# Kernel tuning notes

Hardware: AMD Instinct MI355X
Metric: run time of the kernel (lower is better)

## Reference

```python
import jax, jax.numpy as jnp
import numpy as np

V = 28   # len(string.ascii_lowercase + ' #')
D = 32   # embed dim
H = 2    # heads
DH = D // H
B = 64
S = 1024


def _pe(seq_len, d):
    pos = np.arange(seq_len, dtype=np.float32)[:, None]
    div = np.exp(np.arange(0, d, 2, dtype=np.float32) * (-np.log(10000.0) / d))
    pe = np.zeros((seq_len, d), np.float32)
    pe[:, 0::2] = np.sin(pos * div)
    pe[:, 1::2] = np.cos(pos * div)
    return jnp.asarray(pe)


def setup_inputs() -> dict:
    key = jax.random.key(0)
    ks = jax.random.split(key, 12)
    x = jax.random.randint(ks[0], (B, S), 0, V)
    # per-row valid length in [1, S-4] so last 1-index + 3 stays in range (as original assumes)
    lengths = jax.random.randint(ks[1], (B,), 1, S - 3)
    mask = (jnp.arange(S)[None, :] < lengths[:, None]).astype(jnp.float32)[..., None]
    sc = 1.0 / np.sqrt(D)
    emb = jax.random.normal(ks[2], (V, D), jnp.float32)
    wq = jax.random.normal(ks[3], (D, D), jnp.float32) * sc
    wk = jax.random.normal(ks[4], (D, D), jnp.float32) * sc
    wv = jax.random.normal(ks[5], (D, D), jnp.float32) * sc
    bq = jnp.zeros((D,), jnp.float32)
    bk = jnp.zeros((D,), jnp.float32)
    bv = jnp.zeros((D,), jnp.float32)
    wo = jax.random.normal(ks[6], (D, D), jnp.float32) * sc
    bo = jnp.zeros((D,), jnp.float32)
    w_fc = jax.random.normal(ks[7], (V, D), jnp.float32) * sc
    b_fc = jnp.zeros((V,), jnp.float32)
    pe = _pe(S, D)
    return {"x": x, "mask": mask, "emb": emb, "pe": pe,
            "wq": wq, "bq": bq, "wk": wk, "bk": bk, "wv": wv, "bv": bv,
            "wo": wo, "bo": bo, "w_fc": w_fc, "b_fc": b_fc}


def reference(x, mask, emb, pe, wq, bq, wk, bk, wv, bv, wo, bo, w_fc, b_fc):
    Bn, Sn = x.shape
    h = emb[x] + pe[:Sn]                      # [B,S,D]
    m = mask[..., 0]                          # [B,S]
    # vectorized "last valid index" (replaces per-row python loop + .item())
    valid = m > 0
    last = Sn - 1 - jnp.argmax(valid[:, ::-1], axis=1)   # [B]
    pos = jnp.arange(Sn)
    ext = (pos[None, :] > last[:, None]) & (pos[None, :] <= last[:, None] + 3) \
          & (last[:, None] < Sn - 1)
    nm = jnp.where(ext, jnp.float32(1.0), m)  # extended mask [B,S]
    h = h * nm[..., None]
    # multihead self-attention (torch MultiheadAttention, batch_first)
    def heads(t):
        return t.reshape(Bn, Sn, H, DH).transpose(0, 2, 1, 3)  # [B,H,S,DH]
    q = heads(h @ wq.T + bq)
    k = heads(h @ wk.T + bk)
    v = heads(h @ wv.T + bv)
    scores = jnp.einsum('bhqd,bhkd->bhqk', q, k) / jnp.sqrt(jnp.float32(DH))
    scores = jnp.where((nm == 0)[:, None, None, :], jnp.float32(-1e9), scores)
    a = jax.nn.softmax(scores, axis=-1)
    o = jnp.einsum('bhqk,bhkd->bhqd', a, v).transpose(0, 2, 1, 3).reshape(Bn, Sn, D)
    o = o @ wo.T + bo
    return o @ w_fc.T + b_fc                  # [B,S,V]
```

## Files before the change

kernel.cpp:

```cpp
#include <hip/hip_runtime.h>
#include <math.h>

#define BB 64
#define SS 1024
#define DD 32
#define HH 2
#define DHH 16
#define VV 28
#define QSC 0.3606737602222409f

typedef __attribute__((ext_vector_type(8))) short bf16x8;
typedef __attribute__((ext_vector_type(4))) float f32x4;

__device__ __forceinline__ unsigned pack_hi2(float a, float b) {
    return __builtin_amdgcn_perm(__float_as_uint(b), __float_as_uint(a), 0x07060302u);
}
__device__ __forceinline__ float trunc_hi(float a) {
    return __uint_as_float(__float_as_uint(a) & 0xFFFF0000u);
}
__device__ __forceinline__ unsigned bf_rtne_u(float x) {
    unsigned u = __float_as_uint(x);
    return (u + 0x7FFFu + ((u >> 16) & 1u)) >> 16;
}
__device__ __forceinline__ unsigned pack_rtne2(float a, float b) {
    return bf_rtne_u(a) | (bf_rtne_u(b) << 16);
}
__device__ __forceinline__ bf16x8 as_bf16x8(uint4 u) {
    union { uint4 u; bf16x8 v; } cv; cv.u = u; return cv.v;
}


__global__ __launch_bounds__(256) void k_pre(
        const int* __restrict__ x, const float* __restrict__ mask,
        const float* __restrict__ emb, const float* __restrict__ pe,
        const float* __restrict__ wq, const float* __restrict__ bq,
        const float* __restrict__ wk, const float* __restrict__ bk,
        const float* __restrict__ wv, const float* __restrict__ bv,
        const float* __restrict__ wo, const float* __restrict__ bo,
        const float* __restrict__ wfc, const float* __restrict__ bfc,
        int* __restrict__ e, float* __restrict__ W2, float* __restrict__ b2,
        char* __restrict__ qf, char* __restrict__ kf, char* __restrict__ vf) {
    int bid = blockIdx.x;
    int tid = threadIdx.x;
    if (bid < 1024) {
        __shared__ __align__(16) char hbuf[10240];
        __shared__ __align__(16) float Cb[4][16 * 17];
        char* hHi = hbuf;
        char* hLo = hbuf + 5120;
        int wave = tid >> 6, lane = tid & 63;
        int c = lane & 15, kq = lane >> 4;
        {
            int tt = tid >> 2, q4 = tid & 3;
            int idx = bid * 64 + tt;
            int b = idx >> 10, s = idx & 1023;
            float nm = (mask[b * SS + (s >= 3 ? s - 3 : 0)] != 0.0f) ? 1.0f : 0.0f;
            int tok = x[idx];
            float h[8];
#pragma unroll
            for (int i = 0; i < 8; i++)
                h[i] = (emb[tok * DD + q4 * 8 + i] + pe[s * DD + q4 * 8 + i]) * nm;
            unsigned wh[4], wl[4];
#pragma unroll
            for (int wd = 0; wd < 4; wd++) {
                float a0 = h[2 * wd], a1 = h[2 * wd + 1];
                wh[wd] = pack_hi2(a0, a1);
                wl[wd] = pack_hi2(a0 - trunc_hi(a0), a1 - trunc_hi(a1));
            }
            *(uint4*)(hHi + tt * 80 + q4 * 16) = uint4{wh[0], wh[1], wh[2], wh[3]};
            *(uint4*)(hLo + tt * 80 + q4 * 16) = uint4{wl[0], wl[1], wl[2], wl[3]};
        }
        __syncthreads();
        bf16x8 aHh, aHl;
        {
            int off = (wave * 16 + c) * 80 + kq * 16;
            aHh = *(const bf16x8*)(hHi + off);
            aHl = *(const bf16x8*)(hLo + off);
        }
        int blk_b = bid >> 4;
        int s_w = ((bid * 64) & 1023) + wave * 16;
        const f32x4 z4 = {0.0f, 0.0f, 0.0f, 0.0f};
#pragma unroll
        for (int M = 0; M < 3; M++) {
            const float* W    = M == 0 ? wq : (M == 1 ? wk : wv);
            const float* bias = M == 0 ? bq : (M == 1 ? bk : bv);
            bf16x8 Bh[2], Bl[2];
            float bv_[2];
#pragma unroll
            for (int nt = 0; nt < 2; nt++) {
                const float* wrow = W + (nt * 16 + c) * DD + kq * 8;
                float4 wa = ((const float4*)wrow)[0];
                float4 wb = ((const float4*)wrow)[1];
                float f[8] = {wa.x, wa.y, wa.z, wa.w, wb.x, wb.y, wb.z, wb.w};
                unsigned uh[4], ul[4];
#pragma unroll
                for (int wd = 0; wd < 4; wd++) {
                    float a0 = f[2 * wd], a1 = f[2 * wd + 1];
                    uh[wd] = pack_hi2(a0, a1);
                    ul[wd] = pack_hi2(a0 - trunc_hi(a0), a1 - trunc_hi(a1));
                }
                Bh[nt] = as_bf16x8(uint4{uh[0], uh[1], uh[2], uh[3]});
                Bl[nt] = as_bf16x8(uint4{ul[0], ul[1], ul[2], ul[3]});
                bv_[nt] = bias[nt * 16 + c];
            }
#pragma unroll
            for (int nt = 0; nt < 2; nt++) {
                f32x4 acc = __builtin_amdgcn_mfma_f32_16x16x32_bf16(aHh, Bh[nt], z4, 0, 0, 0);
                acc = __builtin_amdgcn_mfma_f32_16x16x32_bf16(aHl, Bh[nt], acc, 0, 0, 0);
                acc = __builtin_amdgcn_mfma_f32_16x16x32_bf16(aHh, Bl[nt], acc, 0, 0, 0);
#pragma unroll
                for (int r = 0; r < 4; r++) {
                    float val = acc[r] + bv_[nt];
                    if (M == 0) val *= QSC;
                    Cb[wave][(kq * 4 + r) * 17 + c] = val;
                }
                int bh = blk_b * 2 + nt;
                if (M == 0) {
                    int tile = s_w >> 4;
                    int qd = lane >> 4, cc = lane & 15;
                    float f[8];
#pragma unroll
                    for (int j = 0; j < 8; j++) f[j] = Cb[wave][cc * 17 + (qd & 1) * 8 + j];
                    unsigned u[4];
                    if (qd < 2) {
#pragma unroll
                        for (int wd = 0; wd < 4; wd++) u[wd] = pack_hi2(f[2 * wd], f[2 * wd + 1]);
                    } else {
#pragma unroll
                        for (int wd = 0; wd < 4; wd++) {
                            float a0 = f[2 * wd] - trunc_hi(f[2 * wd]);
                            float a1 = f[2 * wd + 1] - trunc_hi(f[2 * wd + 1]);
                            u[wd] = pack_hi2(a0, a1);
                        }
                    }
                    *(uint4*)(qf + ((size_t)((bh << 6) + tile) << 10) + lane * 16)
                        = uint4{u[0], u[1], u[2], u[3]};
                } else if (M == 1) {
                    int cl = lane & 3, qd = (lane >> 2) & 3, t = lane >> 4;
                    int ch = s_w >> 7, g1 = (s_w >> 6) & 1, c0 = (s_w & 63) >> 2;
                    int keyl = 4 * cl + t;
                    float f[8];
#pragma unroll
                    for (int j = 0; j < 8; j++) f[j] = Cb[wave][keyl * 17 + (qd & 1) * 8 + j];
                    unsigned uh[4];
#pragma unroll
                    for (int wd = 0; wd < 4; wd++) uh[wd] = pack_rtne2(f[2 * wd], f[2 * wd + 1]);
                    char* base = kf + ((size_t)((bh << 3) + ch) << 13)
                               + ((g1 << 2) + t) * 1024 + qd * 256 + (c0 + cl) * 16;
                    *(uint4*)(base) = uint4{uh[0], uh[1], uh[2], uh[3]};
                } else if (lane < 32) {
                    int gg = (s_w >> 6) & 15, Qs = (s_w >> 4) & 3;
                    int qrel = lane >> 4, dh = lane & 15;
                    unsigned u[4];
#pragma unroll
                    for (int wd = 0; wd < 4; wd++) {
                        float f0 = Cb[wave][(qrel * 8 + 2 * wd) * 17 + dh];
                        float f1 = Cb[wave][(qrel * 8 + 2 * wd + 1) * 17 + dh];
                        u[wd] = pack_rtne2(f0, f1);
                    }
                    *(uint4*)(vf + ((size_t)((bh << 5) + (gg << 1) + qrel) << 10)
                              + (Qs * 16 + dh) * 16)
                        = uint4{u[0], u[1], u[2], u[3]};
                }
            }
        }
    } else if (bid < 1088) {
        int b = bid - 1024;
        int lm = -1;
        for (int s = tid; s < SS; s += 256)
            if (mask[b * SS + s] != 0.0f) lm = s;
        __shared__ int red[256];
        red[tid] = lm;
        __syncthreads();
        for (int off = 128; off > 0; off >>= 1) {
            if (tid < off) red[tid] = max(red[tid], red[tid + off]);
            __syncthreads();
        }
        if (tid == 0) {
            int last = red[0];
            int ee = last;
            if (last < SS - 1) ee = min(last + 3, SS - 1);
            e[b] = ee;
        }
    } else {
        for (int t2 = tid; t2 < VV * DD + VV; t2 += 256) {
            if (t2 < VV * DD) {
                int vv = t2 / DD, i = t2 % DD;
                float a = 0.0f;
                for (int j = 0; j < DD; j++) a += wfc[vv * DD + j] * wo[j * DD + i];
                W2[t2] = a;
            } else {
                int vv = t2 - VV * DD;
                float a = bfc[vv];
                for (int j = 0; j < DD; j++) a += wfc[vv * DD + j] * bo[j];
                b2[vv] = a;
            }
        }
    }
}

__global__ __launch_bounds__(256) void k_attn_fc(
        const char* __restrict__ qf, const char* __restrict__ kf,
        const char* __restrict__ vf, const int* __restrict__ e,
        const float* __restrict__ W2, const float* __restrict__ b2,
        float* __restrict__ out) {
    __shared__ __align__(16) float Ob[32 * 36];
    __shared__ __align__(16) float sW[VV * 36];
    __shared__ float sb[VV];
    int tid = threadIdx.x;
    int f = blockIdx.x + (blockIdx.y << 5);
    int b = ((f & 7) << 3) + ((f >> 3) & 7);
    int qt = f >> 6;

    for (int i = tid; i < VV * DD; i += 256) sW[(i >> 5) * 36 + (i & 31)] = W2[i];
    if (tid < VV) sb[tid] = b2[tid];

    int kmax = e[b] + 1;
    int ng = (kmax + 63) >> 6;

    int wave = tid >> 6, lane = tid & 63, quad = lane >> 4, c = lane & 15;
    int h = wave & 1, ts = wave >> 1;
    int tile = (qt << 1) + ts;
    int bh = b * 2 + h;

    const char* kbase = kf + ((size_t)(bh << 3) << 13);
    const char* vbase = vf + ((size_t)bh << 15);

    bf16x8 aQ = *(const bf16x8*)(qf + ((size_t)((bh << 6) + tile) << 10) + lane * 16);
    const f32x4 z4 = {0.0f, 0.0f, 0.0f, 0.0f};
    f32x4 accO = z4;
    float l_ = 0.0f;

    for (int g = 0; g < ng; g++) {
        const char* kg = kbase + (size_t)g * 4096;
        const char* vg = vbase + (size_t)g * 2048;
        bf16x8 bv0 = *(const bf16x8*)(vg + lane * 16);
        bf16x8 bv1 = *(const bf16x8*)(vg + 1024 + lane * 16);
        f32x4 st[4];
#pragma unroll
        for (int t = 0; t < 4; t++) {
            bf16x8 aK = *(const bf16x8*)(kg + t * 1024 + lane * 16);
            st[t] = __builtin_amdgcn_mfma_f32_16x16x32_bf16(aK, aQ, z4, 0, 0, 0);
        }
        if (((g + 1) << 6) > kmax) {
            int kb = (g << 6) + (quad << 4);
#pragma unroll
            for (int t = 0; t < 4; t++)
#pragma unroll
                for (int r = 0; r < 4; r++)
                    if (kb + 4 * r + t >= kmax) st[t][r] = -3e38f;
        }
        float p[4][4];
#pragma unroll
        for (int t = 0; t < 4; t++)
#pragma unroll
            for (int r = 0; r < 4; r++) p[t][r] = exp2f(st[t][r]);
#pragma unroll
        for (int t = 0; t < 4; t++)
            l_ += (p[t][0] + p[t][1]) + (p[t][2] + p[t][3]);
        bf16x8 pa0 = as_bf16x8(uint4{pack_hi2(p[0][0], p[1][0]), pack_hi2(p[2][0], p[3][0]),
                                     pack_hi2(p[0][1], p[1][1]), pack_hi2(p[2][1], p[3][1])});
        bf16x8 pa1 = as_bf16x8(uint4{pack_hi2(p[0][2], p[1][2]), pack_hi2(p[2][2], p[3][2]),
                                     pack_hi2(p[0][3], p[1][3]), pack_hi2(p[2][3], p[3][3])});
        accO = __builtin_amdgcn_mfma_f32_16x16x32_bf16(pa0, bv0, accO, 0, 0, 0);
        accO = __builtin_amdgcn_mfma_f32_16x16x32_bf16(pa1, bv1, accO, 0, 0, 0);
    }

    l_ += __shfl_xor(l_, 16);
    l_ += __shfl_xor(l_, 32);

    float* obr = Ob + (ts * 16 + quad * 4) * 36 + h * 16 + c;
#pragma unroll
    for (int r = 0; r < 4; r++) {
        float lr = __shfl(l_, (quad << 2) + r, 16);
        obr[r * 36] = accO[r] * __builtin_amdgcn_rcpf(lr);
    }
    __syncthreads();

    int rl = tid >> 3, j = tid & 7;
    if (j < 7) {
        const float* orow = Ob + rl * 36;
        float ov[DD];
#pragma unroll
        for (int i = 0; i < DD; i += 4) {
            float4 t4 = *(const float4*)(orow + i);
            ov[i] = t4.x; ov[i + 1] = t4.y; ov[i + 2] = t4.z; ov[i + 3] = t4.w;
        }
        int v0 = j << 2;
        float res[4];
#pragma unroll
        for (int k = 0; k < 4; k++) {
            int vv = v0 + k;
            float a = sb[vv];
#pragma unroll
            for (int d = 0; d < DD; d += 4) {
                float4 w4 = *(const float4*)(sW + vv * 36 + d);
                a += ov[d] * w4.x + ov[d + 1] * w4.y + ov[d + 2] * w4.z + ov[d + 3] * w4.w;
            }
            res[k] = a;
        }
        int q = (qt << 5) + rl;
        size_t off = ((size_t)((b << 10) + q)) * VV + v0;
        *(float4*)(out + off) = float4{res[0], res[1], res[2], res[3]};
    }
}

extern "C" void kernel_launch(void* const* d_in, const int* in_sizes, int n_in,
                              void* d_out, int out_size, void* d_ws, size_t ws_size,
                              hipStream_t stream) {
    const int*   x    = (const int*)d_in[0];
    const float* mask = (const float*)d_in[1];
    const float* emb  = (const float*)d_in[2];
    const float* pe   = (const float*)d_in[3];
    const float* wq   = (const float*)d_in[4];
    const float* bq   = (const float*)d_in[5];
    const float* wk   = (const float*)d_in[6];
    const float* bk   = (const float*)d_in[7];
    const float* wv   = (const float*)d_in[8];
    const float* bv   = (const float*)d_in[9];
    const float* wo   = (const float*)d_in[10];
    const float* bo   = (const float*)d_in[11];
    const float* wfc  = (const float*)d_in[12];
    const float* bfc  = (const float*)d_in[13];
    float* out = (float*)d_out;

    char* ws = (char*)d_ws;
    int*   e  = (int*)ws;
    float* W2 = (float*)(ws + 256);
    float* b2 = (float*)(ws + 3840);
    char*  qf = ws + 4096;
    char*  kf = qf + (size_t)8388608;
    char*  vf = kf + (size_t)8388608;

    hipLaunchKernelGGL(k_pre, dim3(1089), dim3(256), 0, stream,
                       x, mask, emb, pe, wq, bq, wk, bk, wv, bv, wo, bo, wfc, bfc,
                       e, W2, b2, qf, kf, vf);
    hipLaunchKernelGGL(k_attn_fc, dim3(SS / 32, BB), dim3(256), 0, stream,
                       qf, kf, vf, e, W2, b2, out);
}
```

Baseline: 138.6 us.

## Process two query tiles per wave and double-buffer K/V register prefetch

```diff
diff --git a/kernel.cpp b/kernel.cpp
--- a/kernel.cpp
+++ b/kernel.cpp
@@ -198,18 +198,77 @@
     }
 }
 
-__global__ __launch_bounds__(256) void k_attn_fc(
+
+#define PREF(K0, K1, K2, K3, V0, V1, GN) {                                         \
+    int gg_ = (GN) < ng ? (GN) : ng - 1;                                           \
+    const char* kg_ = kbase + (size_t)gg_ * 4096;                                  \
+    const char* vg_ = vbase + (size_t)gg_ * 2048;                                  \
+    K0 = *(const bf16x8*)(kg_ + lane * 16);                                        \
+    K1 = *(const bf16x8*)(kg_ + 1024 + lane * 16);                                 \
+    K2 = *(const bf16x8*)(kg_ + 2048 + lane * 16);                                 \
+    K3 = *(const bf16x8*)(kg_ + 3072 + lane * 16);                                 \
+    V0 = *(const bf16x8*)(vg_ + lane * 16);                                        \
+    V1 = *(const bf16x8*)(vg_ + 1024 + lane * 16);                                 \
+}
+
+#define COMP(K0, K1, K2, K3, V0, V1, G) {                                          \
+    f32x4 s0[4], s1[4];                                                            \
+    s0[0] = __builtin_amdgcn_mfma_f32_16x16x32_bf16(K0, aQ0, z4, 0, 0, 0);         \
+    s1[0] = __builtin_amdgcn_mfma_f32_16x16x32_bf16(K0, aQ1, z4, 0, 0, 0);         \
+    s0[1] = __builtin_amdgcn_mfma_f32_16x16x32_bf16(K1, aQ0, z4, 0, 0, 0);         \
+    s1[1] = __builtin_amdgcn_mfma_f32_16x16x32_bf16(K1, aQ1, z4, 0, 0, 0);         \
+    s0[2] = __builtin_amdgcn_mfma_f32_16x16x32_bf16(K2, aQ0, z4, 0, 0, 0);         \
+    s1[2] = __builtin_amdgcn_mfma_f32_16x16x32_bf16(K2, aQ1, z4, 0, 0, 0);         \
+    s0[3] = __builtin_amdgcn_mfma_f32_16x16x32_bf16(K3, aQ0, z4, 0, 0, 0);         \
+    s1[3] = __builtin_amdgcn_mfma_f32_16x16x32_bf16(K3, aQ1, z4, 0, 0, 0);         \
+    if ((((G) + 1) << 6) > kmax) {                                                 \
+        int kb = ((G) << 6) + (quad << 4);                                         \
+        _Pragma("unroll")                                                          \
+        for (int t = 0; t < 4; t++)                                                \
+            _Pragma("unroll")                                                      \
+            for (int r = 0; r < 4; r++)                                            \
+                if (kb + 4 * r + t >= kmax) { s0[t][r] = -3e38f; s1[t][r] = -3e38f; } \
+    }                                                                              \
+    float p0[4][4], p1[4][4];                                                      \
+    _Pragma("unroll")                                                              \
+    for (int t = 0; t < 4; t++)                                                    \
+        _Pragma("unroll")                                                          \
+        for (int r = 0; r < 4; r++) {                                              \
+            p0[t][r] = exp2f(s0[t][r]);                                            \
+            p1[t][r] = exp2f(s1[t][r]);                                            \
+        }                                                                          \
+    _Pragma("unroll")                                                              \
+    for (int t = 0; t < 4; t++) {                                                  \
+        l0 += (p0[t][0] + p0[t][1]) + (p0[t][2] + p0[t][3]);                       \
+        l1 += (p1[t][0] + p1[t][1]) + (p1[t][2] + p1[t][3]);                       \
+    }                                                                              \
+    bf16x8 pa;                                                                     \
+    pa = as_bf16x8(uint4{pack_hi2(p0[0][0], p0[1][0]), pack_hi2(p0[2][0], p0[3][0]), \
+                         pack_hi2(p0[0][1], p0[1][1]), pack_hi2(p0[2][1], p0[3][1])}); \
+    acc0 = __builtin_amdgcn_mfma_f32_16x16x32_bf16(pa, V0, acc0, 0, 0, 0);         \
+    pa = as_bf16x8(uint4{pack_hi2(p0[0][2], p0[1][2]), pack_hi2(p0[2][2], p0[3][2]), \
+                         pack_hi2(p0[0][3], p0[1][3]), pack_hi2(p0[2][3], p0[3][3])}); \
+    acc0 = __builtin_amdgcn_mfma_f32_16x16x32_bf16(pa, V1, acc0, 0, 0, 0);         \
+    pa = as_bf16x8(uint4{pack_hi2(p1[0][0], p1[1][0]), pack_hi2(p1[2][0], p1[3][0]), \
+                         pack_hi2(p1[0][1], p1[1][1]), pack_hi2(p1[2][1], p1[3][1])}); \
+    acc1 = __builtin_amdgcn_mfma_f32_16x16x32_bf16(pa, V0, acc1, 0, 0, 0);         \
+    pa = as_bf16x8(uint4{pack_hi2(p1[0][2], p1[1][2]), pack_hi2(p1[2][2], p1[3][2]), \
+                         pack_hi2(p1[0][3], p1[1][3]), pack_hi2(p1[2][3], p1[3][3])}); \
+    acc1 = __builtin_amdgcn_mfma_f32_16x16x32_bf16(pa, V1, acc1, 0, 0, 0);         \
+}
+
+__global__ __launch_bounds__(256, 3) void k_attn_fc(
         const char* __restrict__ qf, const char* __restrict__ kf,
         const char* __restrict__ vf, const int* __restrict__ e,
         const float* __restrict__ W2, const float* __restrict__ b2,
         float* __restrict__ out) {
-    __shared__ __align__(16) float Ob[32 * 36];
+    __shared__ __align__(16) float Ob[64 * 36];
     __shared__ __align__(16) float sW[VV * 36];
     __shared__ float sb[VV];
     int tid = threadIdx.x;
-    int f = blockIdx.x + (blockIdx.y << 5);
+    int f = blockIdx.x + (blockIdx.y << 4);
     int b = ((f & 7) << 3) + ((f >> 3) & 7);
-    int qt = f >> 6;
+    int qg = f >> 6;
 
     for (int i = tid; i < VV * DD; i += 256) sW[(i >> 5) * 36 + (i & 31)] = W2[i];
     if (tid < VV) sb[tid] = b2[tid];
@@ -218,89 +277,74 @@
     int ng = (kmax + 63) >> 6;
 
     int wave = tid >> 6, lane = tid & 63, quad = lane >> 4, c = lane & 15;
-    int h = wave & 1, ts = wave >> 1;
-    int tile = (qt << 1) + ts;
+    int h = wave & 1, tp = wave >> 1;
+    int t0 = (qg << 2) + (tp << 1);
     int bh = b * 2 + h;
 
     const char* kbase = kf + ((size_t)(bh << 3) << 13);
     const char* vbase = vf + ((size_t)bh << 15);
 
-    bf16x8 aQ = *(const bf16x8*)(qf + ((size_t)((bh << 6) + tile) << 10) + lane * 16);
+    bf16x8 aQ0 = *(const bf16x8*)(qf + ((size_t)((bh << 6) + t0) << 10) + lane * 16);
+    bf16x8 aQ1 = *(const bf16x8*)(qf + ((size_t)((bh << 6) + t0 + 1) << 10) + lane * 16);
     const f32x4 z4 = {0.0f, 0.0f, 0.0f, 0.0f};
-    f32x4 accO = z4;
-    float l_ = 0.0f;
-
-    for (int g = 0; g < ng; g++) {
-        const char* kg = kbase + (size_t)g * 4096;
-        const char* vg = vbase + (size_t)g * 2048;
-        bf16x8 bv0 = *(const bf16x8*)(vg + lane * 16);
-        bf16x8 bv1 = *(const bf16x8*)(vg + 1024 + lane * 16);
-        f32x4 st[4];
-#pragma unroll
-        for (int t = 0; t < 4; t++) {
-            bf16x8 aK = *(const bf16x8*)(kg + t * 1024 + lane * 16);
-            st[t] = __builtin_amdgcn_mfma_f32_16x16x32_bf16(aK, aQ, z4, 0, 0, 0);
-        }
-        if (((g + 1) << 6) > kmax) {
-            int kb = (g << 6) + (quad << 4);
-#pragma unroll
-            for (int t = 0; t < 4; t++)
-#pragma unroll
-                for (int r = 0; r < 4; r++)
-                    if (kb + 4 * r + t >= kmax) st[t][r] = -3e38f;
-        }
-        float p[4][4];
-#pragma unroll
-        for (int t = 0; t < 4; t++)
-#pragma unroll
-            for (int r = 0; r < 4; r++) p[t][r] = exp2f(st[t][r]);
-#pragma unroll
-        for (int t = 0; t < 4; t++)
-            l_ += (p[t][0] + p[t][1]) + (p[t][2] + p[t][3]);
-        bf16x8 pa0 = as_bf16x8(uint4{pack_hi2(p[0][0], p[1][0]), pack_hi2(p[2][0], p[3][0]),
-                                     pack_hi2(p[0][1], p[1][1]), pack_hi2(p[2][1], p[3][1])});
-        bf16x8 pa1 = as_bf16x8(uint4{pack_hi2(p[0][2], p[1][2]), pack_hi2(p[2][2], p[3][2]),
-                                     pack_hi2(p[0][3], p[1][3]), pack_hi2(p[2][3], p[3][3])});
-        accO = __builtin_amdgcn_mfma_f32_16x16x32_bf16(pa0, bv0, accO, 0, 0, 0);
-        accO = __builtin_amdgcn_mfma_f32_16x16x32_bf16(pa1, bv1, accO, 0, 0, 0);
+    f32x4 acc0 = z4, acc1 = z4;
+    float l0 = 0.0f, l1 = 0.0f;
+
+    bf16x8 Ak0, Ak1, Ak2, Ak3, Av0, Av1;
+    bf16x8 Bk0, Bk1, Bk2, Bk3, Bv0, Bv1;
+    PREF(Ak0, Ak1, Ak2, Ak3, Av0, Av1, 0);
+    int g = 0;
+    for (; g + 2 <= ng; g += 2) {
+        PREF(Bk0, Bk1, Bk2, Bk3, Bv0, Bv1, g + 1);
+        COMP(Ak0, Ak1, Ak2, Ak3, Av0, Av1, g);
+        PREF(Ak0, Ak1, Ak2, Ak3, Av0, Av1, g + 2);
+        COMP(Bk0, Bk1, Bk2, Bk3, Bv0, Bv1, g + 1);
     }
-
-    l_ += __shfl_xor(l_, 16);
-    l_ += __shfl_xor(l_, 32);
-
-    float* obr = Ob + (ts * 16 + quad * 4) * 36 + h * 16 + c;
+    if (g < ng) { COMP(Ak0, Ak1, Ak2, Ak3, Av0, Av1, g); }
+
+    l0 += __shfl_xor(l0, 16); l0 += __shfl_xor(l0, 32);
+    l1 += __shfl_xor(l1, 16); l1 += __shfl_xor(l1, 32);
+
+    float* ob0 = Ob + (((tp << 1) << 4) + (quad << 2)) * 36 + (h << 4) + c;
+    float* ob1 = ob0 + 16 * 36;
 #pragma unroll
     for (int r = 0; r < 4; r++) {
-        float lr = __shfl(l_, (quad << 2) + r, 16);
-        obr[r * 36] = accO[r] * __builtin_amdgcn_rcpf(lr);
+        float lr0 = __shfl(l0, (quad << 2) + r, 16);
+        float lr1 = __shfl(l1, (quad << 2) + r, 16);
+        ob0[r * 36] = acc0[r] * __builtin_amdgcn_rcpf(lr0);
+        ob1[r * 36] = acc1[r] * __builtin_amdgcn_rcpf(lr1);
     }
     __syncthreads();
 
     int rl = tid >> 3, j = tid & 7;
     if (j < 7) {
-        const float* orow = Ob + rl * 36;
-        float ov[DD];
-#pragma unroll
-        for (int i = 0; i < DD; i += 4) {
-            float4 t4 = *(const float4*)(orow + i);
-            ov[i] = t4.x; ov[i + 1] = t4.y; ov[i + 2] = t4.z; ov[i + 3] = t4.w;
-        }
         int v0 = j << 2;
-        float res[4];
-#pragma unroll
-        for (int k = 0; k < 4; k++) {
-            int vv = v0 + k;
-            float a = sb[vv];
-#pragma unroll
-            for (int d = 0; d < DD; d += 4) {
-                float4 w4 = *(const float4*)(sW + vv * 36 + d);
-                a += ov[d] * w4.x + ov[d + 1] * w4.y + ov[d + 2] * w4.z + ov[d + 3] * w4.w;
-            }
-            res[k] = a;
-        }
-        int q = (qt << 5) + rl;
-        size_t off = ((size_t)((b << 10) + q)) * VV + v0;
-        *(float4*)(out + off) = float4{res[0], res[1], res[2], res[3]};
+#pragma unroll
+        for (int pass = 0; pass < 2; pass++) {
+            int row = (pass << 5) + rl;
+            const float* orow = Ob + row * 36;
+            float ov[DD];
+#pragma unroll
+            for (int i = 0; i < DD; i += 4) {
+                float4 t4 = *(const float4*)(orow + i);
+                ov[i] = t4.x; ov[i + 1] = t4.y; ov[i + 2] = t4.z; ov[i + 3] = t4.w;
+            }
+            float res[4];
+#pragma unroll
+            for (int k = 0; k < 4; k++) {
+                int vv = v0 + k;
+                float a = sb[vv];
+#pragma unroll
+                for (int d = 0; d < DD; d += 4) {
+                    float4 w4 = *(const float4*)(sW + vv * 36 + d);
+                    a += ov[d] * w4.x + ov[d + 1] * w4.y + ov[d + 2] * w4.z + ov[d + 3] * w4.w;
+                }
+                res[k] = a;
+            }
+            int q = (qg << 6) + row;
+            size_t off = ((size_t)((b << 10) + q)) * VV + v0;
+            *(float4*)(out + off) = float4{res[0], res[1], res[2], res[3]};
+        }
     }
 }
 
@@ -334,6 +378,6 @@
     hipLaunchKernelGGL(k_pre, dim3(1089), dim3(256), 0, stream,
                        x, mask, emb, pe, wq, bq, wk, bk, wv, bv, wo, bo, wfc, bfc,
                        e, W2, b2, qf, kf, vf);
-    hipLaunchKernelGGL(k_attn_fc, dim3(SS / 32, BB), dim3(256), 0, stream,
+    hipLaunchKernelGGL(k_attn_fc, dim3(16, BB), dim3(256), 0, stream,
                        qf, kf, vf, e, W2, b2, out);
 }
```

After: 149.9 us. 8.2% more time.

## Double-buffer K loads in attention loop and simplify block-to-batch mapping

Applied to the files above, without the earlier changes.

```diff
diff --git a/kernel.cpp b/kernel.cpp
--- a/kernel.cpp
+++ b/kernel.cpp
@@ -198,6 +198,49 @@
     }
 }
 
+
+#define LOADK(P0, P1, P2, P3, GN) {                                                \
+    int gg_ = (GN) < ng ? (GN) : ng - 1;                                           \
+    const char* kg_ = kbase + (size_t)gg_ * 4096;                                  \
+    P0 = *(const bf16x8*)(kg_ + lane * 16);                                        \
+    P1 = *(const bf16x8*)(kg_ + 1024 + lane * 16);                                 \
+    P2 = *(const bf16x8*)(kg_ + 2048 + lane * 16);                                 \
+    P3 = *(const bf16x8*)(kg_ + 3072 + lane * 16);                                 \
+}
+
+#define STEP(K0, K1, K2, K3, G) {                                                  \
+    const char* vg_ = vbase + (size_t)(G) * 2048;                                  \
+    bf16x8 v0_ = *(const bf16x8*)(vg_ + lane * 16);                                \
+    bf16x8 v1_ = *(const bf16x8*)(vg_ + 1024 + lane * 16);                         \
+    f32x4 st[4];                                                                   \
+    st[0] = __builtin_amdgcn_mfma_f32_16x16x32_bf16(K0, aQ, z4, 0, 0, 0);          \
+    st[1] = __builtin_amdgcn_mfma_f32_16x16x32_bf16(K1, aQ, z4, 0, 0, 0);          \
+    st[2] = __builtin_amdgcn_mfma_f32_16x16x32_bf16(K2, aQ, z4, 0, 0, 0);          \
+    st[3] = __builtin_amdgcn_mfma_f32_16x16x32_bf16(K3, aQ, z4, 0, 0, 0);          \
+    if ((((G) + 1) << 6) > kmax) {                                                 \
+        int kb = ((G) << 6) + (quad << 4);                                         \
+        _Pragma("unroll")                                                          \
+        for (int t = 0; t < 4; t++)                                                \
+            _Pragma("unroll")                                                      \
+            for (int r = 0; r < 4; r++)                                            \
+                if (kb + 4 * r + t >= kmax) st[t][r] = -3e38f;                     \
+    }                                                                              \
+    float p[4][4];                                                                 \
+    _Pragma("unroll")                                                              \
+    for (int t = 0; t < 4; t++)                                                    \
+        _Pragma("unroll")                                                          \
+        for (int r = 0; r < 4; r++) p[t][r] = __builtin_amdgcn_exp2f(st[t][r]);    \
+    _Pragma("unroll")                                                              \
+    for (int t = 0; t < 4; t++)                                                    \
+        l_ += (p[t][0] + p[t][1]) + (p[t][2] + p[t][3]);                           \
+    bf16x8 pa0 = as_bf16x8(uint4{pack_hi2(p[0][0], p[1][0]), pack_hi2(p[2][0], p[3][0]), \
+                                 pack_hi2(p[0][1], p[1][1]), pack_hi2(p[2][1], p[3][1])}); \
+    bf16x8 pa1 = as_bf16x8(uint4{pack_hi2(p[0][2], p[1][2]), pack_hi2(p[2][2], p[3][2]), \
+                                 pack_hi2(p[0][3], p[1][3]), pack_hi2(p[2][3], p[3][3])}); \
+    accO = __builtin_amdgcn_mfma_f32_16x16x32_bf16(pa0, v0_, accO, 0, 0, 0);       \
+    accO = __builtin_amdgcn_mfma_f32_16x16x32_bf16(pa1, v1_, accO, 0, 0, 0);       \
+}
+
 __global__ __launch_bounds__(256) void k_attn_fc(
         const char* __restrict__ qf, const char* __restrict__ kf,
         const char* __restrict__ vf, const int* __restrict__ e,
@@ -207,9 +250,7 @@
     __shared__ __align__(16) float sW[VV * 36];
     __shared__ float sb[VV];
     int tid = threadIdx.x;
-    int f = blockIdx.x + (blockIdx.y << 5);
-    int b = ((f & 7) << 3) + ((f >> 3) & 7);
-    int qt = f >> 6;
+    int qt = blockIdx.x, b = blockIdx.y;
 
     for (int i = tid; i < VV * DD; i += 256) sW[(i >> 5) * 36 + (i & 31)] = W2[i];
     if (tid < VV) sb[tid] = b2[tid];
@@ -230,40 +271,16 @@
     f32x4 accO = z4;
     float l_ = 0.0f;
 
-    for (int g = 0; g < ng; g++) {
-        const char* kg = kbase + (size_t)g * 4096;
-        const char* vg = vbase + (size_t)g * 2048;
-        bf16x8 bv0 = *(const bf16x8*)(vg + lane * 16);
-        bf16x8 bv1 = *(const bf16x8*)(vg + 1024 + lane * 16);
-        f32x4 st[4];
-#pragma unroll
-        for (int t = 0; t < 4; t++) {
-            bf16x8 aK = *(const bf16x8*)(kg + t * 1024 + lane * 16);
-            st[t] = __builtin_amdgcn_mfma_f32_16x16x32_bf16(aK, aQ, z4, 0, 0, 0);
-        }
-        if (((g + 1) << 6) > kmax) {
-            int kb = (g << 6) + (quad << 4);
-#pragma unroll
-            for (int t = 0; t < 4; t++)
-#pragma unroll
-                for (int r = 0; r < 4; r++)
-                    if (kb + 4 * r + t >= kmax) st[t][r] = -3e38f;
-        }
-        float p[4][4];
-#pragma unroll
-        for (int t = 0; t < 4; t++)
-#pragma unroll
-            for (int r = 0; r < 4; r++) p[t][r] = exp2f(st[t][r]);
-#pragma unroll
-        for (int t = 0; t < 4; t++)
-            l_ += (p[t][0] + p[t][1]) + (p[t][2] + p[t][3]);
-        bf16x8 pa0 = as_bf16x8(uint4{pack_hi2(p[0][0], p[1][0]), pack_hi2(p[2][0], p[3][0]),
-                                     pack_hi2(p[0][1], p[1][1]), pack_hi2(p[2][1], p[3][1])});
-        bf16x8 pa1 = as_bf16x8(uint4{pack_hi2(p[0][2], p[1][2]), pack_hi2(p[2][2], p[3][2]),
-                                     pack_hi2(p[0][3], p[1][3]), pack_hi2(p[2][3], p[3][3])});
-        accO = __builtin_amdgcn_mfma_f32_16x16x32_bf16(pa0, bv0, accO, 0, 0, 0);
-        accO = __builtin_amdgcn_mfma_f32_16x16x32_bf16(pa1, bv1, accO, 0, 0, 0);
+    bf16x8 Ak0, Ak1, Ak2, Ak3, Bk0, Bk1, Bk2, Bk3;
+    LOADK(Ak0, Ak1, Ak2, Ak3, 0);
+    int g = 0;
+    for (; g + 2 <= ng; g += 2) {
+        LOADK(Bk0, Bk1, Bk2, Bk3, g + 1);
+        STEP(Ak0, Ak1, Ak2, Ak3, g);
+        LOADK(Ak0, Ak1, Ak2, Ak3, g + 2);
+        STEP(Bk0, Bk1, Bk2, Bk3, g + 1);
     }
+    if (g < ng) { STEP(Ak0, Ak1, Ak2, Ak3, g); }
 
     l_ += __shfl_xor(l_, 16);
     l_ += __shfl_xor(l_, 32);
```

Result: faster. 120.6 us (-13.0%).
